# Kernel optimization log

Hardware: AMD Instinct MI355X
Metric: run time of the kernel (lower is better)

The kernel has to match this reference:

```python
import jax, jax.numpy as jnp
import numpy as np

B, MN, GN, ME, GE = 1, 40962, 65160, 327660, 163848
MEMB = EEMB = 256
H1, H2 = 512, 64
EPS = 1e-5


def setup_inputs() -> dict:
    key = jax.random.key(0)
    ks = jax.random.split(key, 16)
    s = 0.05
    return {
        "gx": jax.random.normal(ks[0], (B, GN, MEMB), jnp.float32),
        "mx": jax.random.normal(ks[1], (B, MN, MEMB), jnp.float32),
        "me_i": jax.random.randint(ks[2], (2, ME), 0, MN),
        "me_x": jax.random.normal(ks[3], (B, ME, EEMB), jnp.float32),
        "g2me_i": jax.random.randint(ks[4], (2, GE), 0, MN),
        "g2me_x": jax.random.normal(ks[5], (B, GE, EEMB), jnp.float32),
        "m2ge_i": jax.random.randint(ks[6], (2, GE), 0, MN),
        "m2ge_x": jax.random.normal(ks[7], (B, GE, EEMB), jnp.float32),
        # learned params (Linear stored as [in, out]; y = x @ W + b, math-equivalent to torch)
        "W1": jax.random.normal(ks[8], (2 * MEMB + EEMB, H1), jnp.float32) * s,
        "b1": jnp.zeros((H1,), jnp.float32),
        "W2": jax.random.normal(ks[9], (H1, H2), jnp.float32) * s,
        "b2": jnp.zeros((H2,), jnp.float32),
        "W3": jax.random.normal(ks[10], (H2, EEMB), jnp.float32) * s,
        "b3": jnp.zeros((EEMB,), jnp.float32),
        # LayerNorm([m_enum, eemb]) -> elementwise affine over last two dims
        "ln_w": jnp.ones((ME, EEMB), jnp.float32),
        "ln_b": jnp.zeros((ME, EEMB), jnp.float32),
    }


def reference(gx, mx, me_i, me_x, g2me_i, g2me_x, m2ge_i, m2ge_x,
              W1, b1, W2, b2, W3, b3, ln_w, ln_b):
    row, col = me_i[0], me_i[1]
    # gather sender/receiver mesh-node features per edge: [B, ME, 2*MEMB+EEMB]
    h = jnp.concatenate([mx[:, row], mx[:, col], me_x], axis=-1)
    h = jax.nn.silu(h @ W1 + b1)
    h = jax.nn.silu(h @ W2 + b2)
    h = h @ W3 + b3
    # LayerNorm over the last TWO dims (m_enum, eemb), as nn.LayerNorm([m_enum, eemb])
    mean = jnp.mean(h, axis=(-2, -1), keepdims=True)
    var = jnp.var(h, axis=(-2, -1), keepdims=True)
    h = (h - mean) * jax.lax.rsqrt(var + EPS) * ln_w + ln_b
    me_x_new = me_x + h
    return (gx, mx, me_i, me_x_new, g2me_i, g2me_x, m2ge_i, m2ge_x)
```

## Files before the change

### kernel.cpp

```cpp
#include <hip/hip_runtime.h>
#include <hip/hip_bf16.h>

typedef unsigned short u16;
typedef unsigned int u32;
typedef __attribute__((ext_vector_type(8))) short bfrag8;
typedef __attribute__((ext_vector_type(4))) float f32x4;

#define ME_N 327660
#define MN_N 40962
#define MEMB_N 256
#define H1_N 512
#define H2_N 64
#define EEMB_N 256
#define LN_EPS 1e-5f
#define NBLK 5120

static __device__ __forceinline__ u16 f2bf(float f) {
  __hip_bfloat16 h = __float2bfloat16(f);
  return *reinterpret_cast<u16*>(&h);
}
static __device__ __forceinline__ float bf2f(u16 u) {
  union { u32 i; float f; } x; x.i = ((u32)u) << 16; return x.f;
}
static __device__ __forceinline__ u32 pack2(float a, float b) {
  return (u32)f2bf(a) | ((u32)f2bf(b) << 16);
}
static __device__ __forceinline__ float silu_f(float x) {
  return x / (1.0f + __expf(-x));
}
static __device__ __forceinline__ void gload_lds16(const void* g, void* l) {
  __builtin_amdgcn_global_load_lds(
      (const __attribute__((address_space(1))) void*)g,
      (__attribute__((address_space(3))) void*)l, 16, 0, 0);
}

__global__ void i2f_kernel(const int* __restrict__ src, float* __restrict__ dst, int n) {
  int i = blockIdx.x * 256 + threadIdx.x;
  if (i < n) dst[i] = (float)src[i];
}

__global__ void bfconv_kernel(const float* __restrict__ src, u16* __restrict__ dst, int n) {
  int i = (blockIdx.x * 256 + threadIdx.x) * 8;
  if (i >= n) return;
  float4 v0 = reinterpret_cast<const float4*>(src + i)[0];
  float4 v1 = reinterpret_cast<const float4*>(src + i)[1];
  uint4 q;
  q.x = pack2(v0.x, v0.y); q.y = pack2(v0.z, v0.w);
  q.z = pack2(v1.x, v1.y); q.w = pack2(v1.z, v1.w);
  *reinterpret_cast<uint4*>(dst + i) = q;
}

__global__ void wconv1_kernel(const float* __restrict__ src, u16* __restrict__ dst) {
  int i = blockIdx.x * 256 + threadIdx.x;
  if (i >= 512 * 768) return;
  int e   = i & 7;
  int l16 = (i >> 3) & 15;
  int k4  = (i >> 7) & 3;
  int ks  = (i >> 9) & 1;
  int rest = i >> 10;
  int kc = rest % 12;
  int J  = rest / 12;
  int n = J * 16 + l16;
  int k = kc * 64 + ks * 32 + k4 * 8 + e;
  dst[i] = f2bf(src[(size_t)k * 512 + n]);
}

__global__ void wconv_kernel(const float* __restrict__ src, u16* __restrict__ dst,
                             int K, int N) {
  int i = blockIdx.x * 256 + threadIdx.x;
  if (i >= K * N) return;
  int n = i / K;
  int k = i - n * K;
  dst[i] = f2bf(src[(size_t)k * N + n]);
}

__launch_bounds__(512, 2)
__global__ void gemm_fused_kernel(const u16* __restrict__ mxb, const int* __restrict__ me_i,
                                  const float* __restrict__ me_x,
                                  const u16* __restrict__ w1f, const float* __restrict__ b1,
                                  const u16* __restrict__ w2t, const float* __restrict__ b2,
                                  const u16* __restrict__ w3t, const float* __restrict__ b3,
                                  u16* __restrict__ h3, float* __restrict__ partials) {
  __shared__ u16 S[16384];
  __shared__ float red[16];

  const int t = threadIdx.x;
  const int m0 = blockIdx.x * 64;
  const int lane = t & 63;
  const int w = t >> 6;
  const int l16 = lane & 15;
  const int k4 = lane >> 4;
  const int h7 = l16 & 7;

  const int r_st = t >> 3, g_st = t & 7;
  const int gsw = (g_st ^ (r_st & 7)) * 8;
  const int mg = min(m0 + r_st, ME_N - 1);
  const u16* rowr = mxb + (size_t)me_i[mg] * MEMB_N;
  const u16* rowc = mxb + (size_t)me_i[ME_N + mg] * MEMB_N;
  const float* pef = me_x + (size_t)mg * EEMB_N + gsw;

  const f32x4 zero = {0.f, 0.f, 0.f, 0.f};
  f32x4 acc[4][4];
#pragma unroll
  for (int jj = 0; jj < 4; ++jj)
#pragma unroll
    for (int i = 0; i < 4; ++i) acc[jj][i] = zero;

  auto stage_dma = [&](int kcn) {
    const u16* src = (kcn < 4 ? rowr : rowc) + (kcn & 3) * 64 + gsw;
    gload_lds16(src, S + (kcn & 1) * 4096 + w * 512);
  };
  auto loadB = [&](int kc, bfrag8 (&bfr)[2][4]) {
    const u16* wbase = w1f + (size_t)w * 12288 + (size_t)kc * 1024 + k4 * 128 + l16 * 8;
#pragma unroll
    for (int ks = 0; ks < 2; ++ks)
#pragma unroll
      for (int jj = 0; jj < 4; ++jj)
        bfr[ks][jj] = *reinterpret_cast<const bfrag8*>(wbase + (size_t)jj * 98304 + ks * 512);
  };
  auto compute = [&](int kc, const bfrag8 (&bfr)[2][4]) {
    const u16* ab = S + (kc & 1) * 4096;
#pragma unroll
    for (int ks = 0; ks < 2; ++ks) {
      bfrag8 a[4];
#pragma unroll
      for (int i = 0; i < 4; ++i)
        a[i] = *reinterpret_cast<const bfrag8*>(
            &ab[(i * 16 + l16) * 64 + (((ks * 4 + k4) ^ h7) * 8)]);
#pragma unroll
      for (int jj = 0; jj < 4; ++jj)
#pragma unroll
        for (int i = 0; i < 4; ++i)
          acc[jj][i] = __builtin_amdgcn_mfma_f32_16x16x32_bf16(bfr[ks][jj], a[i], acc[jj][i], 0, 0, 0);
    }
  };
  auto packA = [&](const float4& fA, const float4& fB, int slot) {
    uint4 q;
    q.x = pack2(fA.x, fA.y); q.y = pack2(fA.z, fA.w);
    q.z = pack2(fB.x, fB.y); q.w = pack2(fB.z, fB.w);
    *reinterpret_cast<uint4*>(S + slot * 4096 + r_st * 64 + g_st * 8) = q;
  };

  bfrag8 B0[2][4], B1[2][4];
  float4 fA, fB;

  stage_dma(0);
  loadB(0, B0);
#pragma unroll
  for (int kc = 0; kc < 6; kc += 2) {
    loadB(kc + 1, B1);
    stage_dma(kc + 1);
    asm volatile("s_waitcnt vmcnt(9)" ::: "memory");
    __builtin_amdgcn_s_barrier();
    compute(kc, B0);
    __builtin_amdgcn_s_barrier();
    loadB(kc + 2, B0);
    stage_dma(kc + 2);
    asm volatile("s_waitcnt vmcnt(9)" ::: "memory");
    __builtin_amdgcn_s_barrier();
    compute(kc + 1, B1);
    __builtin_amdgcn_s_barrier();
  }
  {
    loadB(7, B1);
    stage_dma(7);
    asm volatile("s_waitcnt vmcnt(9)" ::: "memory");
    __builtin_amdgcn_s_barrier();
    compute(6, B0);
    __builtin_amdgcn_s_barrier();
  }
  {
    fA = reinterpret_cast<const float4*>(pef)[0];
    fB = reinterpret_cast<const float4*>(pef)[1];
    loadB(8, B0);
    asm volatile("s_waitcnt vmcnt(10)" ::: "memory");
    __builtin_amdgcn_s_barrier();
    compute(7, B1);
    packA(fA, fB, 0);
    asm volatile("s_waitcnt lgkmcnt(0)" ::: "memory");
    __builtin_amdgcn_s_barrier();
  }
  {
    fA = reinterpret_cast<const float4*>(pef + 64)[0];
    fB = reinterpret_cast<const float4*>(pef + 64)[1];
    loadB(9, B1);
    compute(8, B0);
    packA(fA, fB, 1);
    asm volatile("s_waitcnt lgkmcnt(0)" ::: "memory");
    __builtin_amdgcn_s_barrier();
  }
  {
    fA = reinterpret_cast<const float4*>(pef + 128)[0];
    fB = reinterpret_cast<const float4*>(pef + 128)[1];
    loadB(10, B0);
    compute(9, B1);
    packA(fA, fB, 0);
    asm volatile("s_waitcnt lgkmcnt(0)" ::: "memory");
    __builtin_amdgcn_s_barrier();
  }
  {
    fA = reinterpret_cast<const float4*>(pef + 192)[0];
    fB = reinterpret_cast<const float4*>(pef + 192)[1];
    loadB(11, B1);
    compute(10, B0);
    packA(fA, fB, 1);
    asm volatile("s_waitcnt lgkmcnt(0)" ::: "memory");
    __builtin_amdgcn_s_barrier();
  }
  {
    compute(11, B1);
  }
  __syncthreads();

  const int kh = w >> 2;
  const int g4 = w & 3;
  const int n2 = g4 * 16 + l16;

  f32x4 acc2p[4];
#pragma unroll
  for (int i = 0; i < 4; ++i) acc2p[i] = zero;

#pragma unroll
  for (int h = 0; h < 2; ++h) {
#pragma unroll
    for (int jr = 0; jr < 2; ++jr) {
      const int jj = 2 * h + jr;
      const float4 bq = *reinterpret_cast<const float4*>(b1 + jj * 128 + w * 16 + k4 * 4);
      const int col = jr * 128 + w * 16 + k4 * 4;
      const int grp = col >> 3, off = col & 7;
#pragma unroll
      for (int i = 0; i < 4; ++i) {
        float x0 = silu_f(acc[jj][i][0] + bq.x);
        float x1 = silu_f(acc[jj][i][1] + bq.y);
        float x2 = silu_f(acc[jj][i][2] + bq.z);
        float x3 = silu_f(acc[jj][i][3] + bq.w);
        uint2 pq = make_uint2(pack2(x0, x1), pack2(x2, x3));
        *reinterpret_cast<uint2*>(&S[(i * 16 + l16) * 256 + ((grp ^ h7) * 8 + off)]) = pq;
      }
    }
    __syncthreads();
    if (kh == h) {
#pragma unroll
      for (int ksl = 0; ksl < 8; ++ksl) {
        bfrag8 w2f = *reinterpret_cast<const bfrag8*>(
            w2t + (size_t)n2 * 512 + kh * 256 + ksl * 32 + k4 * 8);
#pragma unroll
        for (int i = 0; i < 4; ++i) {
          bfrag8 a2 = *reinterpret_cast<const bfrag8*>(
              &S[(i * 16 + l16) * 256 + (((ksl * 4 + k4) ^ h7) * 8)]);
          acc2p[i] = __builtin_amdgcn_mfma_f32_16x16x32_bf16(w2f, a2, acc2p[i], 0, 0, 0);
        }
      }
    }
    __syncthreads();
  }

  float* LDSf = reinterpret_cast<float*>(S);
  u16* h2T = S + 12288;
  if (kh == 1) {
#pragma unroll
    for (int i = 0; i < 4; ++i)
      *reinterpret_cast<f32x4*>(&LDSf[((g4 * 4 + i) * 64 + lane) * 4]) = acc2p[i];
  }
  __syncthreads();
  if (kh == 0) {
    const float4 b2q = *reinterpret_cast<const float4*>(b2 + g4 * 16 + k4 * 4);
    const int col = g4 * 16 + k4 * 4;
    const int grp = col >> 3, off = col & 7;
#pragma unroll
    for (int i = 0; i < 4; ++i) {
      f32x4 o = *reinterpret_cast<f32x4*>(&LDSf[((g4 * 4 + i) * 64 + lane) * 4]);
      float x0 = silu_f(acc2p[i][0] + o[0] + b2q.x);
      float x1 = silu_f(acc2p[i][1] + o[1] + b2q.y);
      float x2 = silu_f(acc2p[i][2] + o[2] + b2q.z);
      float x3 = silu_f(acc2p[i][3] + o[3] + b2q.w);
      uint2 pq = make_uint2(pack2(x0, x1), pack2(x2, x3));
      *reinterpret_cast<uint2*>(&h2T[(i * 16 + l16) * 64 + ((grp ^ h7) * 8 + off)]) = pq;
    }
  }
  __syncthreads();

  bfrag8 a3[2][4];
#pragma unroll
  for (int ks = 0; ks < 2; ++ks)
#pragma unroll
    for (int i = 0; i < 4; ++i)
      a3[ks][i] = *reinterpret_cast<const bfrag8*>(
          &h2T[(i * 16 + l16) * 64 + (((ks * 4 + k4) ^ h7) * 8)]);
  bfrag8 w3f[2][2];
#pragma unroll
  for (int j = 0; j < 2; ++j)
#pragma unroll
    for (int ks = 0; ks < 2; ++ks)
      w3f[j][ks] = *reinterpret_cast<const bfrag8*>(
          w3t + (size_t)(w * 32 + j * 16 + l16) * 64 + ks * 32 + k4 * 8);
  __syncthreads();

  f32x4 acc3[2][4];
#pragma unroll
  for (int j = 0; j < 2; ++j)
#pragma unroll
    for (int i = 0; i < 4; ++i) acc3[j][i] = zero;
#pragma unroll
  for (int ks = 0; ks < 2; ++ks)
#pragma unroll
    for (int j = 0; j < 2; ++j)
#pragma unroll
      for (int i = 0; i < 4; ++i)
        acc3[j][i] = __builtin_amdgcn_mfma_f32_16x16x32_bf16(w3f[j][ks], a3[ks][i], acc3[j][i], 0, 0, 0);

  float lsum = 0.f, lsq = 0.f;
#pragma unroll
  for (int j = 0; j < 2; ++j) {
    const float4 b3q = *reinterpret_cast<const float4*>(b3 + w * 32 + j * 16 + k4 * 4);
    const int col = w * 32 + j * 16 + k4 * 4;
    const int grp = col >> 3, off = col & 7;
#pragma unroll
    for (int i = 0; i < 4; ++i) {
      float x0 = acc3[j][i][0] + b3q.x;
      float x1 = acc3[j][i][1] + b3q.y;
      float x2 = acc3[j][i][2] + b3q.z;
      float x3 = acc3[j][i][3] + b3q.w;
      if (m0 + i * 16 + l16 < ME_N) {
        lsum += (x0 + x1) + (x2 + x3);
        lsq += x0 * x0 + x1 * x1 + x2 * x2 + x3 * x3;
      }
      uint2 pq = make_uint2(pack2(x0, x1), pack2(x2, x3));
      *reinterpret_cast<uint2*>(&S[(i * 16 + l16) * 256 + ((grp ^ h7) * 8 + off)]) = pq;
    }
  }
#pragma unroll
  for (int o = 32; o > 0; o >>= 1) {
    lsum += __shfl_down(lsum, o, 64);
    lsq  += __shfl_down(lsq, o, 64);
  }
  if (lane == 0) { red[w] = lsum; red[8 + w] = lsq; }
  __syncthreads();

  {
    u16* dst = h3 + (size_t)(m0 + r_st) * EEMB_N;
#pragma unroll
    for (int q = 0; q < 4; ++q) {
      const int G = q * 8 + g_st;
      uint4 v = *reinterpret_cast<const uint4*>(&S[r_st * 256 + ((G ^ (r_st & 7)) * 8)]);
      *reinterpret_cast<uint4*>(dst + G * 8) = v;
    }
  }
  if (t == 0) {
    float s1 = 0.f, s2 = 0.f;
#pragma unroll
    for (int q = 0; q < 8; ++q) { s1 += red[q]; s2 += red[8 + q]; }
    partials[2 * blockIdx.x] = s1;
    partials[2 * blockIdx.x + 1] = s2;
  }
}

__global__ void reduce_kernel(const float* __restrict__ partials, int n,
                              float* __restrict__ stats) {
  __shared__ float s1[256], s2[256];
  float a = 0.f, b = 0.f;
  for (int i = threadIdx.x; i < n; i += 256) { a += partials[2 * i]; b += partials[2 * i + 1]; }
  s1[threadIdx.x] = a; s2[threadIdx.x] = b;
  __syncthreads();
  for (int off = 128; off > 0; off >>= 1) {
    if ((int)threadIdx.x < off) {
      s1[threadIdx.x] += s1[threadIdx.x + off];
      s2[threadIdx.x] += s2[threadIdx.x + off];
    }
    __syncthreads();
  }
  if (threadIdx.x == 0) {
    double cnt = (double)ME_N * (double)EEMB_N;
    double mean = (double)s1[0] / cnt;
    double var = (double)s2[0] / cnt - mean * mean;
    stats[0] = (float)mean;
    stats[1] = (float)(1.0 / sqrt(var + (double)LN_EPS));
  }
}

__launch_bounds__(256)
__global__ void final_kernel(const u16* __restrict__ h3, const float* __restrict__ me_x,
                             const float* __restrict__ ln_w, const float* __restrict__ ln_b,
                             const float* __restrict__ stats, float* __restrict__ out) {
  const size_t total = (size_t)ME_N * EEMB_N;
  size_t i = ((size_t)blockIdx.x * 256 + threadIdx.x) * 8;
  if (i >= total) return;
  const float mean = stats[0], inv = stats[1];
  uint4 hv = *reinterpret_cast<const uint4*>(h3 + i);
  float h[8];
  h[0] = bf2f((u16)(hv.x & 0xffff)); h[1] = bf2f((u16)(hv.x >> 16));
  h[2] = bf2f((u16)(hv.y & 0xffff)); h[3] = bf2f((u16)(hv.y >> 16));
  h[4] = bf2f((u16)(hv.z & 0xffff)); h[5] = bf2f((u16)(hv.z >> 16));
  h[6] = bf2f((u16)(hv.w & 0xffff)); h[7] = bf2f((u16)(hv.w >> 16));
  float4 m0 = reinterpret_cast<const float4*>(me_x + i)[0];
  float4 m1 = reinterpret_cast<const float4*>(me_x + i)[1];
  float4 w0 = reinterpret_cast<const float4*>(ln_w + i)[0];
  float4 w1 = reinterpret_cast<const float4*>(ln_w + i)[1];
  float4 c0 = reinterpret_cast<const float4*>(ln_b + i)[0];
  float4 c1 = reinterpret_cast<const float4*>(ln_b + i)[1];
  float4 o0, o1;
  o0.x = m0.x + (h[0] - mean) * inv * w0.x + c0.x;
  o0.y = m0.y + (h[1] - mean) * inv * w0.y + c0.y;
  o0.z = m0.z + (h[2] - mean) * inv * w0.z + c0.z;
  o0.w = m0.w + (h[3] - mean) * inv * w0.w + c0.w;
  o1.x = m1.x + (h[4] - mean) * inv * w1.x + c1.x;
  o1.y = m1.y + (h[5] - mean) * inv * w1.y + c1.y;
  o1.z = m1.z + (h[6] - mean) * inv * w1.z + c1.z;
  o1.w = m1.w + (h[7] - mean) * inv * w1.w + c1.w;
  reinterpret_cast<float4*>(out + i)[0] = o0;
  reinterpret_cast<float4*>(out + i)[1] = o1;
}

extern "C" void kernel_launch(void* const* d_in, const int* in_sizes, int n_in,
                              void* d_out, int out_size, void* d_ws, size_t ws_size,
                              hipStream_t stream) {
  const float* mx   = (const float*)d_in[1];
  const int*   me_i = (const int*)d_in[2];
  const float* me_x = (const float*)d_in[3];
  const float* W1 = (const float*)d_in[8];
  const float* b1 = (const float*)d_in[9];
  const float* W2 = (const float*)d_in[10];
  const float* b2 = (const float*)d_in[11];
  const float* W3 = (const float*)d_in[12];
  const float* b3 = (const float*)d_in[13];
  const float* ln_w = (const float*)d_in[14];
  const float* ln_b = (const float*)d_in[15];

  char* ws = (char*)d_ws;
  u16* w1f = (u16*)(ws + 0);
  u16* w2t = (u16*)(ws + 786432);
  u16* w3t = (u16*)(ws + 851968);
  u16* mxb = (u16*)(ws + 884736);
  u16* h3  = (u16*)(ws + 21857280);
  float* partials = (float*)(ws + 189629440);
  float* stats    = (float*)(ws + 189670400);

  size_t off[8]; size_t a = 0;
  for (int i = 0; i < 8; ++i) { off[i] = a; a += (size_t)in_sizes[i]; }

  for (int i = 0; i < 8; ++i) {
    if (i == 3) continue;
    if (i == 2 || i == 4 || i == 6) {
      int n = in_sizes[i];
      i2f_kernel<<<(n + 255) / 256, 256, 0, stream>>>(
          (const int*)d_in[i], (float*)d_out + off[i], n);
    } else {
      hipMemcpyAsync((char*)d_out + off[i] * 4, d_in[i], (size_t)in_sizes[i] * 4,
                     hipMemcpyDeviceToDevice, stream);
    }
  }

  wconv1_kernel<<<(512 * 768 + 255) / 256, 256, 0, stream>>>(W1, w1f);
  wconv_kernel<<<(512 * 64 + 255) / 256, 256, 0, stream>>>(W2, w2t, 512, 64);
  wconv_kernel<<<(64 * 256 + 255) / 256, 256, 0, stream>>>(W3, w3t, 64, 256);
  {
    int n = MN_N * MEMB_N;
    bfconv_kernel<<<(n / 8 + 255) / 256, 256, 0, stream>>>(mx, mxb, n);
  }

  gemm_fused_kernel<<<NBLK, 512, 0, stream>>>(mxb, me_i, me_x, w1f, b1, w2t, b2,
                                              w3t, b3, h3, partials);
  reduce_kernel<<<1, 256, 0, stream>>>(partials, NBLK, stats);

  const size_t total8 = (size_t)ME_N * EEMB_N / 8;
  final_kernel<<<(int)((total8 + 255) / 256), 256, 0, stream>>>(
      h3, me_x, ln_w, ln_b, stats, (float*)d_out + off[3]);
}
```

Measured before the change: 1.042 ms.

## Split fused MLP block work across 16 waves instead of 8

The fused gather+MLP kernel moves from 512 to 1024 threads per block, and each wave now owns half as many output columns in the first GEMM (acc 2x4 instead of 4x4). The second and third GEMMs and the stats reduction are redistributed over the 16 waves. Only the first 8 waves issue the gather DMA, and the wait counts are adjusted to match. The aim is to cut per-thread register pressure so more waves fit per CU and hide latency better, at the cost of more barrier participants and redundant A-fragment LDS reads per wave.

```diff
diff --git a/kernel.cpp b/kernel.cpp
--- a/kernel.cpp
+++ b/kernel.cpp
@@ -74,7 +74,7 @@
   dst[i] = f2bf(src[(size_t)k * N + n]);
 }
 
-__launch_bounds__(512, 2)
+__launch_bounds__(1024, 4)
 __global__ void gemm_fused_kernel(const u16* __restrict__ mxb, const int* __restrict__ me_i,
                                   const float* __restrict__ me_x,
                                   const u16* __restrict__ w1f, const float* __restrict__ b1,
@@ -82,7 +82,7 @@
                                   const u16* __restrict__ w3t, const float* __restrict__ b3,
                                   u16* __restrict__ h3, float* __restrict__ partials) {
   __shared__ u16 S[16384];
-  __shared__ float red[16];
+  __shared__ float red[32];
 
   const int t = threadIdx.x;
   const int m0 = blockIdx.x * 64;
@@ -92,33 +92,42 @@
   const int k4 = lane >> 4;
   const int h7 = l16 & 7;
 
-  const int r_st = t >> 3, g_st = t & 7;
+  const int r_st = (t >> 3) & 63;
+  const int g_st = t & 7;
   const int gsw = (g_st ^ (r_st & 7)) * 8;
   const int mg = min(m0 + r_st, ME_N - 1);
   const u16* rowr = mxb + (size_t)me_i[mg] * MEMB_N;
   const u16* rowc = mxb + (size_t)me_i[ME_N + mg] * MEMB_N;
-  const float* pef = me_x + (size_t)mg * EEMB_N + gsw;
+
+  const int r4 = t >> 4;
+  const int sub = t & 15;
+  const int sgrp = sub >> 1, shalf = sub & 1;
+  const int mg4 = min(m0 + r4, ME_N - 1);
+  const float* pef = me_x + (size_t)mg4 * EEMB_N + ((sgrp ^ (r4 & 7)) * 8 + shalf * 4);
+  const int doff = r4 * 64 + sgrp * 8 + shalf * 4;
 
   const f32x4 zero = {0.f, 0.f, 0.f, 0.f};
-  f32x4 acc[4][4];
-#pragma unroll
-  for (int jj = 0; jj < 4; ++jj)
+  f32x4 acc[2][4];
+#pragma unroll
+  for (int jj = 0; jj < 2; ++jj)
 #pragma unroll
     for (int i = 0; i < 4; ++i) acc[jj][i] = zero;
 
   auto stage_dma = [&](int kcn) {
-    const u16* src = (kcn < 4 ? rowr : rowc) + (kcn & 3) * 64 + gsw;
-    gload_lds16(src, S + (kcn & 1) * 4096 + w * 512);
+    if (w < 8) {
+      const u16* src = (kcn < 4 ? rowr : rowc) + (kcn & 3) * 64 + gsw;
+      gload_lds16(src, S + (kcn & 1) * 4096 + w * 512);
+    }
   };
-  auto loadB = [&](int kc, bfrag8 (&bfr)[2][4]) {
-    const u16* wbase = w1f + (size_t)w * 12288 + (size_t)kc * 1024 + k4 * 128 + l16 * 8;
+  auto loadB = [&](int kc, bfrag8 (&bfr)[2][2]) {
+    const u16* wbase = w1f + (size_t)(w * 2) * 12288 + (size_t)kc * 1024 + k4 * 128 + l16 * 8;
 #pragma unroll
     for (int ks = 0; ks < 2; ++ks)
 #pragma unroll
-      for (int jj = 0; jj < 4; ++jj)
-        bfr[ks][jj] = *reinterpret_cast<const bfrag8*>(wbase + (size_t)jj * 98304 + ks * 512);
+      for (int jj = 0; jj < 2; ++jj)
+        bfr[ks][jj] = *reinterpret_cast<const bfrag8*>(wbase + (size_t)jj * 12288 + ks * 512);
   };
-  auto compute = [&](int kc, const bfrag8 (&bfr)[2][4]) {
+  auto compute = [&](int kc, const bfrag8 (&bfr)[2][2]) {
     const u16* ab = S + (kc & 1) * 4096;
 #pragma unroll
     for (int ks = 0; ks < 2; ++ks) {
@@ -128,82 +137,80 @@
         a[i] = *reinterpret_cast<const bfrag8*>(
             &ab[(i * 16 + l16) * 64 + (((ks * 4 + k4) ^ h7) * 8)]);
 #pragma unroll
-      for (int jj = 0; jj < 4; ++jj)
+      for (int jj = 0; jj < 2; ++jj)
 #pragma unroll
         for (int i = 0; i < 4; ++i)
           acc[jj][i] = __builtin_amdgcn_mfma_f32_16x16x32_bf16(bfr[ks][jj], a[i], acc[jj][i], 0, 0, 0);
     }
   };
-  auto packA = [&](const float4& fA, const float4& fB, int slot) {
-    uint4 q;
-    q.x = pack2(fA.x, fA.y); q.y = pack2(fA.z, fA.w);
-    q.z = pack2(fB.x, fB.y); q.w = pack2(fB.z, fB.w);
-    *reinterpret_cast<uint4*>(S + slot * 4096 + r_st * 64 + g_st * 8) = q;
+  auto packA = [&](const float4& fq, int slot) {
+    uint2 pq = make_uint2(pack2(fq.x, fq.y), pack2(fq.z, fq.w));
+    *reinterpret_cast<uint2*>(S + slot * 4096 + doff) = pq;
   };
-
-  bfrag8 B0[2][4], B1[2][4];
-  float4 fA, fB;
+  auto waitv = [&]() {
+    if (w < 8) { asm volatile("s_waitcnt vmcnt(5)" ::: "memory"); }
+    else       { asm volatile("s_waitcnt vmcnt(4)" ::: "memory"); }
+  };
+
+  bfrag8 B0[2][2], B1[2][2];
+  float4 fq;
 
   stage_dma(0);
   loadB(0, B0);
 #pragma unroll
-  for (int kc = 0; kc < 6; kc += 2) {
-    loadB(kc + 1, B1);
-    stage_dma(kc + 1);
-    asm volatile("s_waitcnt vmcnt(9)" ::: "memory");
-    __builtin_amdgcn_s_barrier();
-    compute(kc, B0);
-    __builtin_amdgcn_s_barrier();
-    loadB(kc + 2, B0);
-    stage_dma(kc + 2);
-    asm volatile("s_waitcnt vmcnt(9)" ::: "memory");
-    __builtin_amdgcn_s_barrier();
-    compute(kc + 1, B1);
+  for (int kcp = 0; kcp < 6; kcp += 2) {
+    loadB(kcp + 1, B1);
+    stage_dma(kcp + 1);
+    waitv();
+    __builtin_amdgcn_s_barrier();
+    compute(kcp, B0);
+    __builtin_amdgcn_s_barrier();
+    loadB(kcp + 2, B0);
+    stage_dma(kcp + 2);
+    waitv();
+    __builtin_amdgcn_s_barrier();
+    compute(kcp + 1, B1);
     __builtin_amdgcn_s_barrier();
   }
   {
     loadB(7, B1);
     stage_dma(7);
-    asm volatile("s_waitcnt vmcnt(9)" ::: "memory");
+    waitv();
     __builtin_amdgcn_s_barrier();
     compute(6, B0);
     __builtin_amdgcn_s_barrier();
   }
   {
-    fA = reinterpret_cast<const float4*>(pef)[0];
-    fB = reinterpret_cast<const float4*>(pef)[1];
+    fq = *reinterpret_cast<const float4*>(pef);
     loadB(8, B0);
-    asm volatile("s_waitcnt vmcnt(10)" ::: "memory");
+    asm volatile("s_waitcnt vmcnt(5)" ::: "memory");
     __builtin_amdgcn_s_barrier();
     compute(7, B1);
-    packA(fA, fB, 0);
+    packA(fq, 0);
     asm volatile("s_waitcnt lgkmcnt(0)" ::: "memory");
     __builtin_amdgcn_s_barrier();
   }
   {
-    fA = reinterpret_cast<const float4*>(pef + 64)[0];
-    fB = reinterpret_cast<const float4*>(pef + 64)[1];
+    fq = *reinterpret_cast<const float4*>(pef + 64);
     loadB(9, B1);
     compute(8, B0);
-    packA(fA, fB, 1);
+    packA(fq, 1);
     asm volatile("s_waitcnt lgkmcnt(0)" ::: "memory");
     __builtin_amdgcn_s_barrier();
   }
   {
-    fA = reinterpret_cast<const float4*>(pef + 128)[0];
-    fB = reinterpret_cast<const float4*>(pef + 128)[1];
+    fq = *reinterpret_cast<const float4*>(pef + 128);
     loadB(10, B0);
     compute(9, B1);
-    packA(fA, fB, 0);
+    packA(fq, 0);
     asm volatile("s_waitcnt lgkmcnt(0)" ::: "memory");
     __builtin_amdgcn_s_barrier();
   }
   {
-    fA = reinterpret_cast<const float4*>(pef + 192)[0];
-    fB = reinterpret_cast<const float4*>(pef + 192)[1];
+    fq = *reinterpret_cast<const float4*>(pef + 192);
     loadB(11, B1);
     compute(10, B0);
-    packA(fA, fB, 1);
+    packA(fq, 1);
     asm volatile("s_waitcnt lgkmcnt(0)" ::: "memory");
     __builtin_amdgcn_s_barrier();
   }
@@ -212,30 +219,32 @@
   }
   __syncthreads();
 
-  const int kh = w >> 2;
-  const int g4 = w & 3;
-  const int n2 = g4 * 16 + l16;
-
-  f32x4 acc2p[4];
-#pragma unroll
-  for (int i = 0; i < 4; ++i) acc2p[i] = zero;
+  const int kh = w >> 3;
+  const int n2s = w & 3;
+  const int ihalf = (w >> 2) & 1;
+  const int n2 = n2s * 16 + l16;
+
+  f32x4 acc2p[2];
+#pragma unroll
+  for (int ii = 0; ii < 2; ++ii) acc2p[ii] = zero;
 
 #pragma unroll
   for (int h = 0; h < 2; ++h) {
-#pragma unroll
-    for (int jr = 0; jr < 2; ++jr) {
-      const int jj = 2 * h + jr;
-      const float4 bq = *reinterpret_cast<const float4*>(b1 + jj * 128 + w * 16 + k4 * 4);
-      const int col = jr * 128 + w * 16 + k4 * 4;
-      const int grp = col >> 3, off = col & 7;
-#pragma unroll
-      for (int i = 0; i < 4; ++i) {
-        float x0 = silu_f(acc[jj][i][0] + bq.x);
-        float x1 = silu_f(acc[jj][i][1] + bq.y);
-        float x2 = silu_f(acc[jj][i][2] + bq.z);
-        float x3 = silu_f(acc[jj][i][3] + bq.w);
-        uint2 pq = make_uint2(pack2(x0, x1), pack2(x2, x3));
-        *reinterpret_cast<uint2*>(&S[(i * 16 + l16) * 256 + ((grp ^ h7) * 8 + off)]) = pq;
+    if (kh == h) {
+#pragma unroll
+      for (int jj = 0; jj < 2; ++jj) {
+        const int colbase = (w & 7) * 32 + jj * 16 + k4 * 4;
+        const float4 bq = *reinterpret_cast<const float4*>(b1 + h * 256 + colbase);
+        const int grp = colbase >> 3, off = colbase & 7;
+#pragma unroll
+        for (int i = 0; i < 4; ++i) {
+          float x0 = silu_f(acc[jj][i][0] + bq.x);
+          float x1 = silu_f(acc[jj][i][1] + bq.y);
+          float x2 = silu_f(acc[jj][i][2] + bq.z);
+          float x3 = silu_f(acc[jj][i][3] + bq.w);
+          uint2 pq = make_uint2(pack2(x0, x1), pack2(x2, x3));
+          *reinterpret_cast<uint2*>(&S[(i * 16 + l16) * 256 + ((grp ^ h7) * 8 + off)]) = pq;
+        }
       }
     }
     __syncthreads();
@@ -243,12 +252,13 @@
 #pragma unroll
       for (int ksl = 0; ksl < 8; ++ksl) {
         bfrag8 w2f = *reinterpret_cast<const bfrag8*>(
-            w2t + (size_t)n2 * 512 + kh * 256 + ksl * 32 + k4 * 8);
-#pragma unroll
-        for (int i = 0; i < 4; ++i) {
+            w2t + (size_t)n2 * 512 + h * 256 + ksl * 32 + k4 * 8);
+#pragma unroll
+        for (int ii = 0; ii < 2; ++ii) {
+          const int i = ihalf * 2 + ii;
           bfrag8 a2 = *reinterpret_cast<const bfrag8*>(
               &S[(i * 16 + l16) * 256 + (((ksl * 4 + k4) ^ h7) * 8)]);
-          acc2p[i] = __builtin_amdgcn_mfma_f32_16x16x32_bf16(w2f, a2, acc2p[i], 0, 0, 0);
+          acc2p[ii] = __builtin_amdgcn_mfma_f32_16x16x32_bf16(w2f, a2, acc2p[ii], 0, 0, 0);
         }
       }
     }
@@ -259,23 +269,25 @@
   u16* h2T = S + 12288;
   if (kh == 1) {
 #pragma unroll
-    for (int i = 0; i < 4; ++i)
-      *reinterpret_cast<f32x4*>(&LDSf[((g4 * 4 + i) * 64 + lane) * 4]) = acc2p[i];
+    for (int ii = 0; ii < 2; ++ii)
+      *reinterpret_cast<f32x4*>(
+          &LDSf[(((n2s * 2 + ihalf) * 2 + ii) * 64 + lane) * 4]) = acc2p[ii];
   }
   __syncthreads();
   if (kh == 0) {
-    const float4 b2q = *reinterpret_cast<const float4*>(b2 + g4 * 16 + k4 * 4);
-    const int col = g4 * 16 + k4 * 4;
-    const int grp = col >> 3, off = col & 7;
-#pragma unroll
-    for (int i = 0; i < 4; ++i) {
-      f32x4 o = *reinterpret_cast<f32x4*>(&LDSf[((g4 * 4 + i) * 64 + lane) * 4]);
-      float x0 = silu_f(acc2p[i][0] + o[0] + b2q.x);
-      float x1 = silu_f(acc2p[i][1] + o[1] + b2q.y);
-      float x2 = silu_f(acc2p[i][2] + o[2] + b2q.z);
-      float x3 = silu_f(acc2p[i][3] + o[3] + b2q.w);
+    const float4 b2q = *reinterpret_cast<const float4*>(b2 + n2s * 16 + k4 * 4);
+    const int grpn = n2s * 2 + (k4 >> 1), offn = (k4 & 1) * 4;
+#pragma unroll
+    for (int ii = 0; ii < 2; ++ii) {
+      const int i = ihalf * 2 + ii;
+      f32x4 o = *reinterpret_cast<f32x4*>(
+          &LDSf[(((n2s * 2 + ihalf) * 2 + ii) * 64 + lane) * 4]);
+      float x0 = silu_f(acc2p[ii][0] + o[0] + b2q.x);
+      float x1 = silu_f(acc2p[ii][1] + o[1] + b2q.y);
+      float x2 = silu_f(acc2p[ii][2] + o[2] + b2q.z);
+      float x3 = silu_f(acc2p[ii][3] + o[3] + b2q.w);
       uint2 pq = make_uint2(pack2(x0, x1), pack2(x2, x3));
-      *reinterpret_cast<uint2*>(&h2T[(i * 16 + l16) * 64 + ((grp ^ h7) * 8 + off)]) = pq;
+      *reinterpret_cast<uint2*>(&h2T[(i * 16 + l16) * 64 + ((grpn ^ h7) * 8 + offn)]) = pq;
     }
   }
   __syncthreads();
@@ -287,46 +299,38 @@
     for (int i = 0; i < 4; ++i)
       a3[ks][i] = *reinterpret_cast<const bfrag8*>(
           &h2T[(i * 16 + l16) * 64 + (((ks * 4 + k4) ^ h7) * 8)]);
-  bfrag8 w3f[2][2];
-#pragma unroll
-  for (int j = 0; j < 2; ++j)
-#pragma unroll
-    for (int ks = 0; ks < 2; ++ks)
-      w3f[j][ks] = *reinterpret_cast<const bfrag8*>(
-          w3t + (size_t)(w * 32 + j * 16 + l16) * 64 + ks * 32 + k4 * 8);
-  __syncthreads();
-
-  f32x4 acc3[2][4];
-#pragma unroll
-  for (int j = 0; j < 2; ++j)
-#pragma unroll
-    for (int i = 0; i < 4; ++i) acc3[j][i] = zero;
+  bfrag8 w3f[2];
 #pragma unroll
   for (int ks = 0; ks < 2; ++ks)
-#pragma unroll
-    for (int j = 0; j < 2; ++j)
-#pragma unroll
-      for (int i = 0; i < 4; ++i)
-        acc3[j][i] = __builtin_amdgcn_mfma_f32_16x16x32_bf16(w3f[j][ks], a3[ks][i], acc3[j][i], 0, 0, 0);
+    w3f[ks] = *reinterpret_cast<const bfrag8*>(
+        w3t + (size_t)(w * 16 + l16) * 64 + ks * 32 + k4 * 8);
+  __syncthreads();
+
+  f32x4 acc3[4];
+#pragma unroll
+  for (int i = 0; i < 4; ++i) acc3[i] = zero;
+#pragma unroll
+  for (int ks = 0; ks < 2; ++ks)
+#pragma unroll
+    for (int i = 0; i < 4; ++i)
+      acc3[i] = __builtin_amdgcn_mfma_f32_16x16x32_bf16(w3f[ks], a3[ks][i], acc3[i], 0, 0, 0);
 
   float lsum = 0.f, lsq = 0.f;
-#pragma unroll
-  for (int j = 0; j < 2; ++j) {
-    const float4 b3q = *reinterpret_cast<const float4*>(b3 + w * 32 + j * 16 + k4 * 4);
-    const int col = w * 32 + j * 16 + k4 * 4;
-    const int grp = col >> 3, off = col & 7;
+  {
+    const float4 b3q = *reinterpret_cast<const float4*>(b3 + w * 16 + k4 * 4);
+    const int grp3 = w * 2 + (k4 >> 1), off3 = (k4 & 1) * 4;
 #pragma unroll
     for (int i = 0; i < 4; ++i) {
-      float x0 = acc3[j][i][0] + b3q.x;
-      float x1 = acc3[j][i][1] + b3q.y;
-      float x2 = acc3[j][i][2] + b3q.z;
-      float x3 = acc3[j][i][3] + b3q.w;
+      float x0 = acc3[i][0] + b3q.x;
+      float x1 = acc3[i][1] + b3q.y;
+      float x2 = acc3[i][2] + b3q.z;
+      float x3 = acc3[i][3] + b3q.w;
       if (m0 + i * 16 + l16 < ME_N) {
         lsum += (x0 + x1) + (x2 + x3);
         lsq += x0 * x0 + x1 * x1 + x2 * x2 + x3 * x3;
       }
       uint2 pq = make_uint2(pack2(x0, x1), pack2(x2, x3));
-      *reinterpret_cast<uint2*>(&S[(i * 16 + l16) * 256 + ((grp ^ h7) * 8 + off)]) = pq;
+      *reinterpret_cast<uint2*>(&S[(i * 16 + l16) * 256 + ((grp3 ^ h7) * 8 + off3)]) = pq;
     }
   }
 #pragma unroll
@@ -334,22 +338,22 @@
     lsum += __shfl_down(lsum, o, 64);
     lsq  += __shfl_down(lsq, o, 64);
   }
-  if (lane == 0) { red[w] = lsum; red[8 + w] = lsq; }
-  __syncthreads();
-
-  {
-    u16* dst = h3 + (size_t)(m0 + r_st) * EEMB_N;
-#pragma unroll
-    for (int q = 0; q < 4; ++q) {
-      const int G = q * 8 + g_st;
-      uint4 v = *reinterpret_cast<const uint4*>(&S[r_st * 256 + ((G ^ (r_st & 7)) * 8)]);
+  if (lane == 0) { red[w] = lsum; red[16 + w] = lsq; }
+  __syncthreads();
+
+  {
+    u16* dst = h3 + (size_t)(m0 + r4) * EEMB_N;
+#pragma unroll
+    for (int q = 0; q < 2; ++q) {
+      const int G = sub * 2 + q;
+      uint4 v = *reinterpret_cast<const uint4*>(&S[r4 * 256 + ((G ^ (r4 & 7)) * 8)]);
       *reinterpret_cast<uint4*>(dst + G * 8) = v;
     }
   }
   if (t == 0) {
     float s1 = 0.f, s2 = 0.f;
 #pragma unroll
-    for (int q = 0; q < 8; ++q) { s1 += red[q]; s2 += red[8 + q]; }
+    for (int q = 0; q < 16; ++q) { s1 += red[q]; s2 += red[16 + q]; }
     partials[2 * blockIdx.x] = s1;
     partials[2 * blockIdx.x + 1] = s2;
   }
@@ -458,8 +462,8 @@
     bfconv_kernel<<<(n / 8 + 255) / 256, 256, 0, stream>>>(mx, mxb, n);
   }
 
-  gemm_fused_kernel<<<NBLK, 512, 0, stream>>>(mxb, me_i, me_x, w1f, b1, w2t, b2,
-                                              w3t, b3, h3, partials);
+  gemm_fused_kernel<<<NBLK, 1024, 0, stream>>>(mxb, me_i, me_x, w1f, b1, w2t, b2,
+                                               w3t, b3, h3, partials);
   reduce_kernel<<<1, 256, 0, stream>>>(partials, NBLK, stats);
 
   const size_t total8 = (size_t)ME_N * EEMB_N / 8;
```

Result: no change. 1.034 ms (-0.8%).
